# Kernel optimization log

Hardware: AMD Instinct MI355X
Metric: run time of the kernel (lower is better)

Reference implementation:

```python
import jax, jax.numpy as jnp
import numpy as np

NH = 16  # num_attention_heads
DH = 64  # attention_head_size
HS = 1024
LN_EPS = 1e-5


def _linear(x, W, b):
    return jnp.einsum('bsh,oh->bso', x, W) + b


def _mha(q, k, v, mask):
    # q:[B,Sq,H] k,v:[B,Sk,H] mask:[B,Sk] int (1=keep,0=mask)
    B, Sq, _ = q.shape
    Sk = k.shape[1]
    qh = q.reshape(B, Sq, NH, DH).transpose(0, 2, 1, 3)
    kh = k.reshape(B, Sk, NH, DH).transpose(0, 2, 1, 3)
    vh = v.reshape(B, Sk, NH, DH).transpose(0, 2, 1, 3)
    scores = jnp.einsum('bhqd,bhkd->bhqk', qh, kh) / np.sqrt(DH).astype(np.float32)
    if mask is not None:
        scores = jnp.where(mask[:, None, None, :] == 0, jnp.float32(-1e9), scores)
    probs = jax.nn.softmax(scores, axis=-1)  # dropout is identity in eval
    ctx = jnp.einsum('bhqk,bhkd->bhqd', probs, vh)
    return ctx.transpose(0, 2, 1, 3).reshape(B, Sq, NH * DH)


def _layernorm(x, g, b):
    mu = jnp.mean(x, axis=-1, keepdims=True)
    var = jnp.mean(jnp.square(x - mu), axis=-1, keepdims=True)
    return (x - mu) * jax.lax.rsqrt(var + LN_EPS) * g + b


def setup_inputs() -> dict:
    key = jax.random.key(0)
    ks = jax.random.split(key, 20)
    B, Sc, Se = 4, 512, 2048
    s = 0.02
    inp = {
        'claim_embeddings': jax.random.normal(ks[0], (B, Sc, HS), jnp.float32),
        'evidence_embeddings': jax.random.normal(ks[1], (B, Se, HS), jnp.float32),
        'claim_mask': jax.random.randint(ks[2], (B, Sc), 0, 2, jnp.int32),
        'evidence_mask': jax.random.randint(ks[3], (B, Se), 0, 2, jnp.int32),
    }
    names = ['cq', 'ek', 'ev', 'eq', 'ck', 'cv']
    for i, n in enumerate(names):
        inp['W_' + n] = jax.random.normal(ks[4 + i], (HS, HS), jnp.float32) * s
        inp['b_' + n] = jnp.zeros((HS,), jnp.float32)
    inp['ln_g'] = jnp.ones((HS,), jnp.float32)
    inp['ln_b'] = jnp.zeros((HS,), jnp.float32)
    return inp


def reference(claim_embeddings, evidence_embeddings, claim_mask, evidence_mask,
              W_cq, b_cq, W_ek, b_ek, W_ev, b_ev,
              W_eq, b_eq, W_ck, b_ck, W_cv, b_cv, ln_g, ln_b):
    claim_att = _mha(_linear(claim_embeddings, W_cq, b_cq),
                     _linear(evidence_embeddings, W_ek, b_ek),
                     _linear(evidence_embeddings, W_ev, b_ev), evidence_mask)
    evid_att = _mha(_linear(evidence_embeddings, W_eq, b_eq),
                    _linear(claim_embeddings, W_ck, b_ck),
                    _linear(claim_embeddings, W_cv, b_cv), claim_mask)
    claim_out = _layernorm(claim_embeddings + claim_att, ln_g, ln_b)
    evid_out = _layernorm(evidence_embeddings + evid_att, ln_g, ln_b)
    return (claim_out, evid_out)
```

## Files before the change

kernel.cpp:

```cpp
#include <hip/hip_runtime.h>
#include <hip/hip_bf16.h>
#include <stdint.h>

typedef __hip_bfloat16 bf16;
typedef __attribute__((ext_vector_type(8))) short bf16x8;
typedef __attribute__((ext_vector_type(4))) float f32x4;

#define DEV __device__ __forceinline__

DEV float lo_bf(unsigned int v) { union { unsigned int u; float f; } c; c.u = v << 16; return c.f; }
DEV float hi_bf(unsigned int v) { union { unsigned int u; float f; } c; c.u = v & 0xffff0000u; return c.f; }

DEV int probe_bf16(const void* ln_g) { return ((const uint16_t*)ln_g)[0] == 0x3F80; }

DEV unsigned short f2bs(float f) { union { bf16 h; unsigned short s; } u; u.h = __float2bfloat16(f); return u.s; }

DEV float ldf(const void* p, size_t i, int bfm) {
    return bfm ? __bfloat162float(((const bf16*)p)[i]) : ((const float*)p)[i];
}

DEV bf16x8 pack8(float4 x, float4 y) {
    union { unsigned short s[8]; bf16x8 v; } u;
    u.s[0] = f2bs(x.x); u.s[1] = f2bs(x.y); u.s[2] = f2bs(x.z); u.s[3] = f2bs(x.w);
    u.s[4] = f2bs(y.x); u.s[5] = f2bs(y.y); u.s[6] = f2bs(y.z); u.s[7] = f2bs(y.w);
    return u.v;
}

DEV bf16x8 ld8cvt(const void* p, size_t i, int bfm) {
    if (bfm) return *(const bf16x8*)((const bf16*)p + i);
    const float4* f = (const float4*)((const float*)p + i);
    return pack8(f[0], f[1]);
}

DEV void gload_lds16(const bf16* g, bf16* l) {
    __builtin_amdgcn_global_load_lds(
        (const __attribute__((address_space(1))) void*)g,
        (__attribute__((address_space(3))) void*)l,
        16, 0, 0);
}

__global__ __launch_bounds__(256) void conv_bf16(
    const void* __restrict__ Xc, const void* __restrict__ Xe,
    const void* __restrict__ W0, const void* __restrict__ W1, const void* __restrict__ W2,
    const void* __restrict__ W3, const void* __restrict__ W4, const void* __restrict__ W5,
    bf16* __restrict__ dst, const void* __restrict__ probe)
{
    const int bfm = probe_bf16(probe);
    const size_t tot = (size_t)16384 * 1024;
    const size_t step = (size_t)gridDim.x * 256 * 8;
    for (size_t e = ((size_t)blockIdx.x * 256 + threadIdx.x) * 8; e < tot; e += step) {
        const size_t row = e >> 10;
        const void* src; size_t off;
        if (row < 2048)       { src = Xc; off = e; }
        else if (row < 10240) { src = Xe; off = e - (size_t)2048 * 1024; }
        else {
            const int wi = (int)((row - 10240) >> 10);
            src = (wi == 0) ? W0 : (wi == 1) ? W1 : (wi == 2) ? W2 :
                  (wi == 3) ? W3 : (wi == 4) ? W4 : W5;
            off = e - (size_t)(10240 + wi * 1024) * 1024;
        }
        *(bf16x8*)(dst + e) = ld8cvt(src, off, bfm);
    }
}

__global__ __launch_bounds__(256) void gemm_fast(
    const bf16* __restrict__ AW,
    const void* __restrict__ B0, const void* __restrict__ B1, const void* __restrict__ B2,
    const void* __restrict__ B3, const void* __restrict__ B4, const void* __restrict__ B5,
    bf16* __restrict__ Out, const void* __restrict__ probe)
{
    __shared__ __align__(16) bf16 As[2][128 * 32];
    __shared__ __align__(16) bf16 Bs[2][128 * 32];

    const int bfm = probe_bf16(probe);
    const int L = (blockIdx.x & 7) * 240 + (blockIdx.x >> 3);
    const int z  = L / 640;
    const int rem = L % 640;
    const int bx = rem >> 3;
    const int by = rem & 7;
    const int rowBase = bx * 128;
    const int colBase = by * 128;
    const int ev = rowBase >= 2048;
    const int widx = z * 2 + ev;

    const bf16* Ap = AW;
    const bf16* Wp = AW + (size_t)(10240 + widx * 1024) * 1024;
    const void* bias = (widx == 0) ? B0 : (widx == 1) ? B1 : (widx == 2) ? B2 :
                       (widx == 3) ? B3 : (widx == 4) ? B4 : B5;
    bf16* O = Out + (size_t)z * 10240 * 1024;

    const int tid  = threadIdx.x;
    const int wave = tid >> 6;
    const int lane = tid & 63;
    const int wm   = wave >> 1;
    const int wn   = wave & 1;
    const int quad = lane >> 4;
    const int l16  = lane & 15;

    f32x4 acc[4][4];
#pragma unroll
    for (int i = 0; i < 4; i++)
#pragma unroll
        for (int j = 0; j < 4; j++) acc[i][j] = (f32x4){0.f, 0.f, 0.f, 0.f};

    const int sr = tid >> 2;
    const int sc = (tid & 3) * 8;
    const size_t ga = (size_t)(rowBase + sr) * 1024 + sc;
    const size_t gb = (size_t)(colBase + sr) * 1024 + sc;

    auto stage = [&](int buf, int k0) {
        gload_lds16(Ap + ga + k0,                     &As[buf][tid * 8]);
        gload_lds16(Ap + ga + (size_t)64 * 1024 + k0, &As[buf][2048 + tid * 8]);
        gload_lds16(Wp + gb + k0,                     &Bs[buf][tid * 8]);
        gload_lds16(Wp + gb + (size_t)64 * 1024 + k0, &Bs[buf][2048 + tid * 8]);
    };

    stage(0, 0);
    __syncthreads();

    int cur = 0;
    for (int k0 = 0; k0 < 1024; k0 += 32) {
        if (k0 + 32 < 1024) stage(cur ^ 1, k0 + 32);

        bf16x8 af[4], bfr[4];
#pragma unroll
        for (int i = 0; i < 4; i++) {
            af[i]  = *(const bf16x8*)(&As[cur][(wm * 64 + i * 16 + l16) * 32 + quad * 8]);
            bfr[i] = *(const bf16x8*)(&Bs[cur][(wn * 64 + i * 16 + l16) * 32 + quad * 8]);
        }
#pragma unroll
        for (int i = 0; i < 4; i++)
#pragma unroll
            for (int j = 0; j < 4; j++)
                acc[i][j] = __builtin_amdgcn_mfma_f32_16x16x32_bf16(af[i], bfr[j], acc[i][j], 0, 0, 0);

        __syncthreads();
        cur ^= 1;
    }

#pragma unroll
    for (int j = 0; j < 4; j++) {
        const int col = colBase + wn * 64 + j * 16 + l16;
        const float bv = ldf(bias, col, bfm);
#pragma unroll
        for (int i = 0; i < 4; i++) {
            const int row0 = rowBase + wm * 64 + i * 16 + quad * 4;
#pragma unroll
            for (int rr = 0; rr < 4; rr++)
                O[(size_t)(row0 + rr) * 1024 + col] = __float2bfloat16(acc[i][j][rr] + bv);
        }
    }
}

DEV void attn_core(const bf16* __restrict__ Q, const bf16* __restrict__ K,
                   const bf16* __restrict__ V, const int* __restrict__ mask,
                   bf16* __restrict__ O, int Sk, int h, int qRow0)
{
    __shared__ __align__(16) short Ks [64 * 72];
    __shared__ __align__(16) short VTs[64 * 72];
    __shared__ __align__(16) short Ps [4][16 * 72];

    const int tid  = threadIdx.x;
    const int w    = tid >> 6;
    const int lane = tid & 63;
    const int quad = lane >> 4;
    const int l16  = lane & 15;
    const int qRow = qRow0 + w * 16 + l16;

    const short* Qp = (const short*)Q + (size_t)qRow * 1024 + h * 64;
    const bf16x8 qf0 = *(const bf16x8*)(Qp + quad * 8);
    const bf16x8 qf1 = *(const bf16x8*)(Qp + 32 + quad * 8);

    f32x4 oacc[4];
#pragma unroll
    for (int dt = 0; dt < 4; dt++) oacc[dt] = (f32x4){0.f, 0.f, 0.f, 0.f};
    float mrun[4] = {-3e38f, -3e38f, -3e38f, -3e38f};
    float lrun[4] = {0.f, 0.f, 0.f, 0.f};

    const int sn = tid >> 2, sseg = tid & 3;
    const int vn = lane,     vdg  = w;

    bf16x8 pk0, pk1, pv0, pv1;
    auto loadkv = [&](int k0) {
        const short* src = (const short*)K + (size_t)(k0 + sn) * 1024 + h * 64 + sseg * 16;
        pk0 = *(const bf16x8*)src;
        pk1 = *(const bf16x8*)(src + 8);
        const short* vsrc = (const short*)V + (size_t)(k0 + vn) * 1024 + h * 64 + vdg * 16;
        pv0 = *(const bf16x8*)vsrc;
        pv1 = *(const bf16x8*)(vsrc + 8);
    };
    loadkv(0);

    for (int k0 = 0; k0 < Sk; k0 += 64) {
        __syncthreads();
        *(bf16x8*)(Ks + sn * 72 + sseg * 16)     = pk0;
        *(bf16x8*)(Ks + sn * 72 + sseg * 16 + 8) = pk1;
#pragma unroll
        for (int i = 0; i < 8; i++) VTs[(vdg * 16 + i) * 72 + vn]     = pv0[i];
#pragma unroll
        for (int i = 0; i < 8; i++) VTs[(vdg * 16 + 8 + i) * 72 + vn] = pv1[i];
        __syncthreads();
        {
            int kn = k0 + 64; if (kn >= Sk) kn = 0;
            loadkv(kn);
        }

        const int mv_all = mask[k0 + lane];

        f32x4 sacc[4];
#pragma unroll
        for (int t = 0; t < 4; t++) {
            const bf16x8 kf0 = *(const bf16x8*)(Ks + (t * 16 + l16) * 72 + quad * 8);
            const bf16x8 kf1 = *(const bf16x8*)(Ks + (t * 16 + l16) * 72 + 32 + quad * 8);
            f32x4 s = (f32x4){0.f, 0.f, 0.f, 0.f};
            s = __builtin_amdgcn_mfma_f32_16x16x32_bf16(qf0, kf0, s, 0, 0, 0);
            s = __builtin_amdgcn_mfma_f32_16x16x32_bf16(qf1, kf1, s, 0, 0, 0);
            const int mv = __shfl(mv_all, t * 16 + l16);
#pragma unroll
            for (int r = 0; r < 4; r++) sacc[t][r] = mv ? s[r] * 0.125f : -1e9f;
        }

        float cmax[4];
#pragma unroll
        for (int r = 0; r < 4; r++)
            cmax[r] = fmaxf(fmaxf(sacc[0][r], sacc[1][r]), fmaxf(sacc[2][r], sacc[3][r]));
#pragma unroll
        for (int m = 1; m < 16; m <<= 1)
#pragma unroll
            for (int r = 0; r < 4; r++) cmax[r] = fmaxf(cmax[r], __shfl_xor(cmax[r], m));

        float alpha[4], rsum[4];
#pragma unroll
        for (int r = 0; r < 4; r++) {
            const float mn = fmaxf(mrun[r], cmax[r]);
            alpha[r] = __expf(mrun[r] - mn);
            mrun[r] = mn;
            rsum[r] = 0.f;
        }
#pragma unroll
        for (int t = 0; t < 4; t++)
#pragma unroll
            for (int r = 0; r < 4; r++) {
                const float p = __expf(sacc[t][r] - mrun[r]);
                rsum[r] += p;
                Ps[w][(quad * 4 + r) * 72 + t * 16 + l16] = f2bs(p);
            }
#pragma unroll
        for (int m = 1; m < 16; m <<= 1)
#pragma unroll
            for (int r = 0; r < 4; r++) rsum[r] += __shfl_xor(rsum[r], m);
#pragma unroll
        for (int r = 0; r < 4; r++) lrun[r] = lrun[r] * alpha[r] + rsum[r];
#pragma unroll
        for (int dt = 0; dt < 4; dt++)
#pragma unroll
            for (int r = 0; r < 4; r++) oacc[dt][r] *= alpha[r];


        const bf16x8 pa0 = *(const bf16x8*)(Ps[w] + l16 * 72 + quad * 8);
        const bf16x8 pa1 = *(const bf16x8*)(Ps[w] + l16 * 72 + 32 + quad * 8);
#pragma unroll
        for (int dt = 0; dt < 4; dt++) {
            const bf16x8 vb0 = *(const bf16x8*)(VTs + (dt * 16 + l16) * 72 + quad * 8);
            const bf16x8 vb1 = *(const bf16x8*)(VTs + (dt * 16 + l16) * 72 + 32 + quad * 8);
            oacc[dt] = __builtin_amdgcn_mfma_f32_16x16x32_bf16(pa0, vb0, oacc[dt], 0, 0, 0);
            oacc[dt] = __builtin_amdgcn_mfma_f32_16x16x32_bf16(pa1, vb1, oacc[dt], 0, 0, 0);
        }
    }

    short* Op = (short*)O;
#pragma unroll
    for (int r = 0; r < 4; r++) {
        const float inv = 1.0f / lrun[r];
        const size_t row = (size_t)(qRow0 + w * 16 + quad * 4 + r) * 1024 + h * 64;
#pragma unroll
        for (int dt = 0; dt < 4; dt++)
            Op[row + dt * 16 + l16] = f2bs(oacc[dt][r] * inv);
    }
}

__global__ __launch_bounds__(256) void attn_flat(
    const bf16* __restrict__ Q1, const bf16* __restrict__ K1, const bf16* __restrict__ V1,
    const int* __restrict__ m1, bf16* __restrict__ O1,
    const bf16* __restrict__ Q2, const bf16* __restrict__ K2, const bf16* __restrict__ V2,
    const int* __restrict__ m2, bf16* __restrict__ O2)
{
    const int xcd = blockIdx.x & 7;
    const int idx = blockIdx.x >> 3;
    const int grp = idx / 5;
    const int pos = idx % 5;

    if (pos == 0) {
        const int j = xcd * 64 + grp;
        const int b = j >> 7;
        const int h = (j >> 3) & 15;
        const int qRow0 = (j & 7) * 64;
        attn_core(Q1 + (size_t)b * 512 * 1024,
                  K1 + (size_t)b * 2048 * 1024,
                  V1 + (size_t)b * 2048 * 1024,
                  m1 + (size_t)b * 2048,
                  O1 + (size_t)b * 512 * 1024, 2048, h, qRow0);
    } else {
        const int j = xcd * 256 + grp * 4 + (pos - 1);
        const int b = j >> 9;
        const int h = (j >> 5) & 15;
        const int qRow0 = (j & 31) * 64;
        attn_core(Q2 + (size_t)b * 2048 * 1024,
                  K2 + (size_t)b * 512 * 1024,
                  V2 + (size_t)b * 512 * 1024,
                  m2 + (size_t)b * 512,
                  O2 + (size_t)b * 2048 * 1024, 512, h, qRow0);
    }
}

__global__ __launch_bounds__(256) void attn_dual(
    const bf16* __restrict__ Q1, const bf16* __restrict__ K1, const bf16* __restrict__ V1,
    const int* __restrict__ m1, bf16* __restrict__ O1,
    const bf16* __restrict__ Q2, const bf16* __restrict__ K2, const bf16* __restrict__ V2,
    const int* __restrict__ m2, bf16* __restrict__ O2)
{
    const int z = blockIdx.z;
    if (z < 4) {
        if (blockIdx.x >= 8) return;
        attn_core(Q1 + (size_t)z * 512 * 1024,
                  K1 + (size_t)z * 2048 * 1024,
                  V1 + (size_t)z * 2048 * 1024,
                  m1 + (size_t)z * 2048,
                  O1 + (size_t)z * 512 * 1024, 2048, blockIdx.y, blockIdx.x * 64);
    } else {
        const int b = z - 4;
        attn_core(Q2 + (size_t)b * 2048 * 1024,
                  K2 + (size_t)b * 512 * 1024,
                  V2 + (size_t)b * 512 * 1024,
                  m2 + (size_t)b * 512,
                  O2 + (size_t)b * 2048 * 1024, 512, blockIdx.y, blockIdx.x * 64);
    }
}

DEV void gemm_core(const void* __restrict__ A, int aRow0,
                   const void* __restrict__ W, const void* __restrict__ bias,
                   bf16* __restrict__ O, int bfm)
{
    __shared__ __align__(16) short As [128 * 40];
    __shared__ __align__(16) short Bsh[128 * 40];

    const int tid  = threadIdx.x;
    const int wave = tid >> 6;
    const int lane = tid & 63;
    const int wm   = wave >> 1;
    const int wn   = wave & 1;
    const int quad = lane >> 4;
    const int l16  = lane & 15;

    const int rowBase = blockIdx.x * 128;
    const int colBase = blockIdx.y * 128;

    f32x4 acc[4][4];
#pragma unroll
    for (int i = 0; i < 4; i++)
#pragma unroll
        for (int j = 0; j < 4; j++) acc[i][j] = (f32x4){0.f, 0.f, 0.f, 0.f};

    const int r  = tid >> 2;
    const int c8 = (tid & 3) * 8;
    const size_t aIdx = (size_t)(aRow0 + rowBase + r) * 1024 + c8;
    const size_t wIdx = (size_t)(colBase + r) * 1024 + c8;
    short* sA0 = As  + r * 40 + c8;
    short* sA1 = As  + (r + 64) * 40 + c8;
    short* sB0 = Bsh + r * 40 + c8;
    short* sB1 = Bsh + (r + 64) * 40 + c8;

    auto compute = [&]() {
        bf16x8 af[4], bfr[4];
#pragma unroll
        for (int i = 0; i < 4; i++) {
            af[i]  = *(const bf16x8*)(As  + (wm * 64 + i * 16 + l16) * 40 + quad * 8);
            bfr[i] = *(const bf16x8*)(Bsh + (wn * 64 + i * 16 + l16) * 40 + quad * 8);
        }
#pragma unroll
        for (int i = 0; i < 4; i++)
#pragma unroll
            for (int j = 0; j < 4; j++)
                acc[i][j] = __builtin_amdgcn_mfma_f32_16x16x32_bf16(af[i], bfr[j], acc[i][j], 0, 0, 0);
    };

    if (bfm) {
        const bf16* Ab = (const bf16*)A;
        const bf16* Wb = (const bf16*)W;
        bf16x8 ra0 = *(const bf16x8*)(Ab + aIdx);
        bf16x8 ra1 = *(const bf16x8*)(Ab + aIdx + (size_t)64 * 1024);
        bf16x8 rb0 = *(const bf16x8*)(Wb + wIdx);
        bf16x8 rb1 = *(const bf16x8*)(Wb + wIdx + (size_t)64 * 1024);
        for (int k0 = 0; k0 < 1024; k0 += 32) {
            __syncthreads();
            *(bf16x8*)sA0 = ra0; *(bf16x8*)sA1 = ra1;
            *(bf16x8*)sB0 = rb0; *(bf16x8*)sB1 = rb1;
            __syncthreads();
            const int kn = (k0 + 32) & 1023;
            ra0 = *(const bf16x8*)(Ab + aIdx + kn);
            ra1 = *(const bf16x8*)(Ab + aIdx + (size_t)64 * 1024 + kn);
            rb0 = *(const bf16x8*)(Wb + wIdx + kn);
            rb1 = *(const bf16x8*)(Wb + wIdx + (size_t)64 * 1024 + kn);
            compute();
        }
    } else {
        const float* Af = (const float*)A;
        const float* Wf = (const float*)W;
        float4 f[4][2];
        auto loadf = [&](int k) {
            f[0][0] = *(const float4*)(Af + aIdx + k);
            f[0][1] = *(const float4*)(Af + aIdx + k + 4);
            f[1][0] = *(const float4*)(Af + aIdx + (size_t)64 * 1024 + k);
            f[1][1] = *(const float4*)(Af + aIdx + (size_t)64 * 1024 + k + 4);
            f[2][0] = *(const float4*)(Wf + wIdx + k);
            f[2][1] = *(const float4*)(Wf + wIdx + k + 4);
            f[3][0] = *(const float4*)(Wf + wIdx + (size_t)64 * 1024 + k);
            f[3][1] = *(const float4*)(Wf + wIdx + (size_t)64 * 1024 + k + 4);
        };
        loadf(0);
        for (int k0 = 0; k0 < 1024; k0 += 32) {
            const bf16x8 ra0 = pack8(f[0][0], f[0][1]);
            const bf16x8 ra1 = pack8(f[1][0], f[1][1]);
            const bf16x8 rb0 = pack8(f[2][0], f[2][1]);
            const bf16x8 rb1 = pack8(f[3][0], f[3][1]);
            __syncthreads();
            *(bf16x8*)sA0 = ra0; *(bf16x8*)sA1 = ra1;
            *(bf16x8*)sB0 = rb0; *(bf16x8*)sB1 = rb1;
            __syncthreads();
            loadf((k0 + 32) & 1023);
            compute();
        }
    }

#pragma unroll
    for (int j = 0; j < 4; j++) {
        const int col = colBase + wn * 64 + j * 16 + l16;
        const float bv = ldf(bias, col, bfm);
#pragma unroll
        for (int i = 0; i < 4; i++) {
            const int row0 = rowBase + wm * 64 + i * 16 + quad * 4;
#pragma unroll
            for (int rr = 0; rr < 4; rr++)
                O[(size_t)(row0 + rr) * 1024 + col] = __float2bfloat16(acc[i][j][rr] + bv);
        }
    }
}

__global__ __launch_bounds__(256) void gemm_bt6(
    const void* __restrict__ Ac, const void* __restrict__ Ae,
    const void* __restrict__ W0, const void* __restrict__ W1, const void* __restrict__ W2,
    const void* __restrict__ W3, const void* __restrict__ W4, const void* __restrict__ W5,
    const void* __restrict__ B0, const void* __restrict__ B1, const void* __restrict__ B2,
    const void* __restrict__ B3, const void* __restrict__ B4, const void* __restrict__ B5,
    bf16* __restrict__ O0, bf16* __restrict__ O1, bf16* __restrict__ O2,
    bf16* __restrict__ O3, bf16* __restrict__ O4, bf16* __restrict__ O5,
    const void* __restrict__ dt_probe)
{
    const int z = blockIdx.z;
    if (z < 3 && blockIdx.x >= 16) return;
    const int bfm = probe_bf16(dt_probe);
    const void* A = (z < 3) ? Ac : Ae;
    const void* W    = (z == 0) ? W0 : (z == 1) ? W1 : (z == 2) ? W2 : (z == 3) ? W3 : (z == 4) ? W4 : W5;
    const void* bias = (z == 0) ? B0 : (z == 1) ? B1 : (z == 2) ? B2 : (z == 3) ? B3 : (z == 4) ? B4 : B5;
    bf16* O          = (z == 0) ? O0 : (z == 1) ? O1 : (z == 2) ? O2 : (z == 3) ? O3 : (z == 4) ? O4 : O5;
    gemm_core(A, 0, W, bias, O, bfm);
}

DEV void ln_body(const void* __restrict__ X, size_t xrow, const bf16* __restrict__ Att,
                 size_t arow, const void* __restrict__ G, const void* __restrict__ Bb,
                 void* __restrict__ O, size_t orow, int bfm)
{
    __shared__ float r1[4], r2[4];
    const int tid = threadIdx.x;
    const size_t abase = arow * 1024 + tid * 4;
    const size_t xbase = xrow * 1024 + tid * 4;
    const uint2 ab = *(const uint2*)(Att + abase);
    const float v0 = ldf(X, xbase + 0, bfm) + lo_bf(ab.x);
    const float v1 = ldf(X, xbase + 1, bfm) + hi_bf(ab.x);
    const float v2 = ldf(X, xbase + 2, bfm) + lo_bf(ab.y);
    const float v3 = ldf(X, xbase + 3, bfm) + hi_bf(ab.y);
    float s  = v0 + v1 + v2 + v3;
    float ss = v0 * v0 + v1 * v1 + v2 * v2 + v3 * v3;
    for (int off = 32; off > 0; off >>= 1) { s += __shfl_down(s, off); ss += __shfl_down(ss, off); }
    if ((tid & 63) == 0) { r1[tid >> 6] = s; r2[tid >> 6] = ss; }
    __syncthreads();
    const float S  = r1[0] + r1[1] + r1[2] + r1[3];
    const float SS = r2[0] + r2[1] + r2[2] + r2[3];
    const float mu   = S * (1.f / 1024.f);
    const float var  = SS * (1.f / 1024.f) - mu * mu;
    const float rstd = rsqrtf(var + 1e-5f);
    const float g0 = ldf(G, tid * 4 + 0, bfm), g1 = ldf(G, tid * 4 + 1, bfm);
    const float g2 = ldf(G, tid * 4 + 2, bfm), g3 = ldf(G, tid * 4 + 3, bfm);
    const float bb0 = ldf(Bb, tid * 4 + 0, bfm), bb1 = ldf(Bb, tid * 4 + 1, bfm);
    const float bb2 = ldf(Bb, tid * 4 + 2, bfm), bb3 = ldf(Bb, tid * 4 + 3, bfm);
    const float o0 = (v0 - mu) * rstd * g0 + bb0;
    const float o1 = (v1 - mu) * rstd * g1 + bb1;
    const float o2 = (v2 - mu) * rstd * g2 + bb2;
    const float o3 = (v3 - mu) * rstd * g3 + bb3;
    const size_t obase = orow * 1024 + tid * 4;
    if (bfm) {
        union { unsigned short s4[4]; uint2 u; } pack;
        pack.s4[0] = f2bs(o0); pack.s4[1] = f2bs(o1); pack.s4[2] = f2bs(o2); pack.s4[3] = f2bs(o3);
        *(uint2*)((bf16*)O + obase) = pack.u;
    } else {
        *(float4*)((float*)O + obase) = (float4){o0, o1, o2, o3};
    }
}

__global__ __launch_bounds__(256) void ln_all(
    const void* __restrict__ Xc, const void* __restrict__ Xe, const bf16* __restrict__ Att,
    const void* __restrict__ G, const void* __restrict__ Bb, void* __restrict__ O)
{
    const int bfm = probe_bf16(G);
    const size_t row = blockIdx.x;
    if (row < 2048) ln_body(Xc, row,        Att, row, G, Bb, O, row, bfm);
    else            ln_body(Xe, row - 2048, Att, row, G, Bb, O, row, bfm);
}

__global__ __launch_bounds__(256) void ln_kernel(
    const void* __restrict__ X, int xRow0, const bf16* __restrict__ Att,
    const void* __restrict__ G, const void* __restrict__ Bb,
    void* __restrict__ O, size_t oRow0)
{
    const int bfm = probe_bf16(G);
    const size_t row = blockIdx.x;
    ln_body(X, (size_t)xRow0 + row, Att, row, G, Bb, O, oRow0 + row, bfm);
}

extern "C" void kernel_launch(void* const* d_in, const int* in_sizes, int n_in,
                              void* d_out, int out_size, void* d_ws, size_t ws_size,
                              hipStream_t stream)
{
    (void)in_sizes; (void)n_in; (void)out_size;

    const void* c_emb  = d_in[0];
    const void* e_emb  = d_in[1];
    const int*  c_mask = (const int*)d_in[2];
    const int*  e_mask = (const int*)d_in[3];
    const void* W_cq = d_in[4];  const void* b_cq = d_in[5];
    const void* W_ek = d_in[6];  const void* b_ek = d_in[7];
    const void* W_ev = d_in[8];  const void* b_ev = d_in[9];
    const void* W_eq = d_in[10]; const void* b_eq = d_in[11];
    const void* W_ck = d_in[12]; const void* b_ck = d_in[13];
    const void* W_cv = d_in[14]; const void* b_cv = d_in[15];
    const void* ln_g = d_in[16]; const void* ln_b = d_in[17];

    const int B = 4, Scl = 512, Sev = 2048;
    const size_t MC = (size_t)B * Scl;
    const size_t ME = (size_t)B * Sev;
    const size_t MT = MC + ME;
    const size_t RW = MT * 1024;

    dim3 blk(256);
    const size_t need_fast = (3 * RW + (size_t)16384 * 1024) * sizeof(bf16);

    if (ws_size >= need_fast) {
        bf16* Qr = (bf16*)d_ws;
        bf16* Kr = Qr + RW;
        bf16* Vr = Kr + RW;
        bf16* CV = Vr + RW;

        conv_bf16<<<dim3(2048), blk, 0, stream>>>(
            c_emb, e_emb, W_cq, W_eq, W_ck, W_ek, W_cv, W_ev, CV, ln_g);

        gemm_fast<<<dim3(1920), blk, 0, stream>>>(
            CV, b_cq, b_eq, b_ck, b_ek, b_cv, b_ev, Qr, ln_g);

        attn_flat<<<dim3(2560), blk, 0, stream>>>(
            Qr,             Kr + MC * 1024, Vr + MC * 1024, e_mask, Qr,
            Qr + MC * 1024, Kr,             Vr,             c_mask, Qr + MC * 1024);

        ln_all<<<dim3((unsigned)MT), blk, 0, stream>>>(
            c_emb, e_emb, Qr, ln_g, ln_b, d_out);
    } else {
        bf16* q_c = (bf16*)d_ws;
        bf16* k_c = q_c + MC * 1024;
        bf16* v_c = k_c + MC * 1024;
        bf16* q_e = v_c + MC * 1024;
        bf16* k_e = q_e + ME * 1024;
        bf16* v_e = k_e + ME * 1024;

        gemm_bt6<<<dim3(64, 8, 6), blk, 0, stream>>>(
            c_emb, e_emb,
            W_cq, W_ck, W_cv, W_eq, W_ek, W_ev,
            b_cq, b_ck, b_cv, b_eq, b_ek, b_ev,
            q_c, k_c, v_c, q_e, k_e, v_e, ln_g);

        attn_dual<<<dim3(32, 16, 8), blk, 0, stream>>>(
            q_c, k_e, v_e, e_mask, q_c,
            q_e, k_c, v_c, c_mask, q_e);

        ln_kernel<<<dim3((unsigned)MC), blk, 0, stream>>>(
            c_emb, 0, q_c, ln_g, ln_b, d_out, 0);
        ln_kernel<<<dim3((unsigned)ME), blk, 0, stream>>>(
            e_emb, 0, q_e, ln_g, ln_b, d_out, MC);
    }
}
```

Baseline: 431.3 us.

## Double-buffer K/V tiles in attention and fold softmax scale into exp2

The attention inner loop now ping-pongs between two shared-memory K and V^T buffers. The next tile is staged after the current PV matmul, so each iteration needs one barrier instead of two. The mask load is prefetched alongside K and V, and the 1/sqrt(d) scale is multiplied by log2(e) so the softmax can use exp2f instead of __expf. The cost is double the K/V LDS footprint, which may lower occupancy.

New measurement: 439.4 us. No clear change (+1.9%).

```diff
diff --git a/kernel.cpp b/kernel.cpp
--- a/kernel.cpp
+++ b/kernel.cpp
@@ -156,8 +156,8 @@
                    const bf16* __restrict__ V, const int* __restrict__ mask,
                    bf16* __restrict__ O, int Sk, int h, int qRow0)
 {
-    __shared__ __align__(16) short Ks [64 * 72];
-    __shared__ __align__(16) short VTs[64 * 72];
+    __shared__ __align__(16) short Ks [2][64 * 72];
+    __shared__ __align__(16) short VTs[2][64 * 72];
     __shared__ __align__(16) short Ps [4][16 * 72];
 
     const int tid  = threadIdx.x;
@@ -181,6 +181,7 @@
     const int vn = lane,     vdg  = w;
 
     bf16x8 pk0, pk1, pv0, pv1;
+    int pm;
     auto loadkv = [&](int k0) {
         const short* src = (const short*)K + (size_t)(k0 + sn) * 1024 + h * 64 + sseg * 16;
         pk0 = *(const bf16x8*)src;
@@ -188,36 +189,40 @@
         const short* vsrc = (const short*)V + (size_t)(k0 + vn) * 1024 + h * 64 + vdg * 16;
         pv0 = *(const bf16x8*)vsrc;
         pv1 = *(const bf16x8*)(vsrc + 8);
+        pm  = mask[k0 + lane];
     };
+    auto stage = [&](int buf) {
+        *(bf16x8*)(Ks[buf] + sn * 72 + sseg * 16)     = pk0;
+        *(bf16x8*)(Ks[buf] + sn * 72 + sseg * 16 + 8) = pk1;
+#pragma unroll
+        for (int i = 0; i < 8; i++) VTs[buf][(vdg * 16 + i) * 72 + vn]     = pv0[i];
+#pragma unroll
+        for (int i = 0; i < 8; i++) VTs[buf][(vdg * 16 + 8 + i) * 72 + vn] = pv1[i];
+    };
+
     loadkv(0);
-
+    stage(0);
+    __syncthreads();
+
+    const float SCL = 0.18033688f;
+
+    int cur = 0;
     for (int k0 = 0; k0 < Sk; k0 += 64) {
-        __syncthreads();
-        *(bf16x8*)(Ks + sn * 72 + sseg * 16)     = pk0;
-        *(bf16x8*)(Ks + sn * 72 + sseg * 16 + 8) = pk1;
-#pragma unroll
-        for (int i = 0; i < 8; i++) VTs[(vdg * 16 + i) * 72 + vn]     = pv0[i];
-#pragma unroll
-        for (int i = 0; i < 8; i++) VTs[(vdg * 16 + 8 + i) * 72 + vn] = pv1[i];
-        __syncthreads();
-        {
-            int kn = k0 + 64; if (kn >= Sk) kn = 0;
-            loadkv(kn);
-        }
-
-        const int mv_all = mask[k0 + lane];
+        const int mv_all = pm;
+        const bool more = (k0 + 64 < Sk);
+        if (more) loadkv(k0 + 64);
 
         f32x4 sacc[4];
 #pragma unroll
         for (int t = 0; t < 4; t++) {
-            const bf16x8 kf0 = *(const bf16x8*)(Ks + (t * 16 + l16) * 72 + quad * 8);
-            const bf16x8 kf1 = *(const bf16x8*)(Ks + (t * 16 + l16) * 72 + 32 + quad * 8);
+            const bf16x8 kf0 = *(const bf16x8*)(Ks[cur] + (t * 16 + l16) * 72 + quad * 8);
+            const bf16x8 kf1 = *(const bf16x8*)(Ks[cur] + (t * 16 + l16) * 72 + 32 + quad * 8);
             f32x4 s = (f32x4){0.f, 0.f, 0.f, 0.f};
             s = __builtin_amdgcn_mfma_f32_16x16x32_bf16(qf0, kf0, s, 0, 0, 0);
             s = __builtin_amdgcn_mfma_f32_16x16x32_bf16(qf1, kf1, s, 0, 0, 0);
             const int mv = __shfl(mv_all, t * 16 + l16);
 #pragma unroll
-            for (int r = 0; r < 4; r++) sacc[t][r] = mv ? s[r] * 0.125f : -1e9f;
+            for (int r = 0; r < 4; r++) sacc[t][r] = mv ? s[r] * SCL : -1e9f;
         }
 
         float cmax[4];
@@ -233,7 +238,7 @@
 #pragma unroll
         for (int r = 0; r < 4; r++) {
             const float mn = fmaxf(mrun[r], cmax[r]);
-            alpha[r] = __expf(mrun[r] - mn);
+            alpha[r] = exp2f(mrun[r] - mn);
             mrun[r] = mn;
             rsum[r] = 0.f;
         }
@@ -241,7 +246,7 @@
         for (int t = 0; t < 4; t++)
 #pragma unroll
             for (int r = 0; r < 4; r++) {
-                const float p = __expf(sacc[t][r] - mrun[r]);
+                const float p = exp2f(sacc[t][r] - mrun[r]);
                 rsum[r] += p;
                 Ps[w][(quad * 4 + r) * 72 + t * 16 + l16] = f2bs(p);
             }
@@ -261,10 +266,16 @@
         const bf16x8 pa1 = *(const bf16x8*)(Ps[w] + l16 * 72 + 32 + quad * 8);
 #pragma unroll
         for (int dt = 0; dt < 4; dt++) {
-            const bf16x8 vb0 = *(const bf16x8*)(VTs + (dt * 16 + l16) * 72 + quad * 8);
-            const bf16x8 vb1 = *(const bf16x8*)(VTs + (dt * 16 + l16) * 72 + 32 + quad * 8);
+            const bf16x8 vb0 = *(const bf16x8*)(VTs[cur] + (dt * 16 + l16) * 72 + quad * 8);
+            const bf16x8 vb1 = *(const bf16x8*)(VTs[cur] + (dt * 16 + l16) * 72 + 32 + quad * 8);
             oacc[dt] = __builtin_amdgcn_mfma_f32_16x16x32_bf16(pa0, vb0, oacc[dt], 0, 0, 0);
             oacc[dt] = __builtin_amdgcn_mfma_f32_16x16x32_bf16(pa1, vb1, oacc[dt], 0, 0, 0);
+        }
+
+        if (more) {
+            stage(cur ^ 1);
+            __syncthreads();
+            cur ^= 1;
         }
     }
 
```

## Process two query tiles per attention block to reuse staged K/V

Applied to the files above, without the earlier changes.

Adds attn_core2, in which each 256-thread block handles 128 query rows (two 64-row tiles per head) and reuses each K/V tile staged in shared memory for both. The flat attention grid is halved and its block-to-work mapping recomputed. This cuts global K/V loads and the shared-memory transpose work per query row, at the cost of more registers (doubled accumulators and softmax state) and fewer blocks to fill the GPU.

New measurement: 454.3 us. 5.3% more time.

```diff
diff --git a/kernel.cpp b/kernel.cpp
--- a/kernel.cpp
+++ b/kernel.cpp
@@ -152,30 +152,39 @@
     }
 }
 
-DEV void attn_core(const bf16* __restrict__ Q, const bf16* __restrict__ K,
-                   const bf16* __restrict__ V, const int* __restrict__ mask,
-                   bf16* __restrict__ O, int Sk, int h, int qRow0)
+DEV void attn_core2(const bf16* __restrict__ Q, const bf16* __restrict__ K,
+                    const bf16* __restrict__ V, const int* __restrict__ mask,
+                    bf16* __restrict__ O, int Sk, int h, int qRow0)
 {
     __shared__ __align__(16) short Ks [64 * 72];
     __shared__ __align__(16) short VTs[64 * 72];
-    __shared__ __align__(16) short Ps [4][16 * 72];
+    __shared__ __align__(16) short Ps [4][2][16 * 72];
 
     const int tid  = threadIdx.x;
     const int w    = tid >> 6;
     const int lane = tid & 63;
     const int quad = lane >> 4;
     const int l16  = lane & 15;
-    const int qRow = qRow0 + w * 16 + l16;
-
-    const short* Qp = (const short*)Q + (size_t)qRow * 1024 + h * 64;
-    const bf16x8 qf0 = *(const bf16x8*)(Qp + quad * 8);
-    const bf16x8 qf1 = *(const bf16x8*)(Qp + 32 + quad * 8);
-
-    f32x4 oacc[4];
-#pragma unroll
-    for (int dt = 0; dt < 4; dt++) oacc[dt] = (f32x4){0.f, 0.f, 0.f, 0.f};
-    float mrun[4] = {-3e38f, -3e38f, -3e38f, -3e38f};
-    float lrun[4] = {0.f, 0.f, 0.f, 0.f};
+
+    bf16x8 qf[2][2];
+#pragma unroll
+    for (int mt = 0; mt < 2; mt++) {
+        const short* Qp = (const short*)Q +
+            (size_t)(qRow0 + mt * 64 + w * 16 + l16) * 1024 + h * 64;
+        qf[mt][0] = *(const bf16x8*)(Qp + quad * 8);
+        qf[mt][1] = *(const bf16x8*)(Qp + 32 + quad * 8);
+    }
+
+    f32x4 oacc[2][4];
+    float mrun[2][4], lrun[2][4];
+#pragma unroll
+    for (int mt = 0; mt < 2; mt++)
+#pragma unroll
+        for (int dt = 0; dt < 4; dt++) {
+            oacc[mt][dt] = (f32x4){0.f, 0.f, 0.f, 0.f};
+            mrun[mt][dt] = -3e38f;
+            lrun[mt][dt] = 0.f;
+        }
 
     const int sn = tid >> 2, sseg = tid & 3;
     const int vn = lane,     vdg  = w;
@@ -207,6 +216,183 @@
 
         const int mv_all = mask[k0 + lane];
 
+        f32x4 sacc[2][4];
+#pragma unroll
+        for (int t = 0; t < 4; t++) {
+            const bf16x8 kf0 = *(const bf16x8*)(Ks + (t * 16 + l16) * 72 + quad * 8);
+            const bf16x8 kf1 = *(const bf16x8*)(Ks + (t * 16 + l16) * 72 + 32 + quad * 8);
+            const int mv = __shfl(mv_all, t * 16 + l16);
+#pragma unroll
+            for (int mt = 0; mt < 2; mt++) {
+                f32x4 s = (f32x4){0.f, 0.f, 0.f, 0.f};
+                s = __builtin_amdgcn_mfma_f32_16x16x32_bf16(qf[mt][0], kf0, s, 0, 0, 0);
+                s = __builtin_amdgcn_mfma_f32_16x16x32_bf16(qf[mt][1], kf1, s, 0, 0, 0);
+#pragma unroll
+                for (int r = 0; r < 4; r++) sacc[mt][t][r] = mv ? s[r] * 0.125f : -1e9f;
+            }
+        }
+
+#pragma unroll
+        for (int mt = 0; mt < 2; mt++) {
+            float cmax[4];
+#pragma unroll
+            for (int r = 0; r < 4; r++)
+                cmax[r] = fmaxf(fmaxf(sacc[mt][0][r], sacc[mt][1][r]),
+                                fmaxf(sacc[mt][2][r], sacc[mt][3][r]));
+#pragma unroll
+            for (int m = 1; m < 16; m <<= 1)
+#pragma unroll
+                for (int r = 0; r < 4; r++) cmax[r] = fmaxf(cmax[r], __shfl_xor(cmax[r], m));
+
+            float alpha[4], rsum[4];
+#pragma unroll
+            for (int r = 0; r < 4; r++) {
+                const float mn = fmaxf(mrun[mt][r], cmax[r]);
+                alpha[r] = __expf(mrun[mt][r] - mn);
+                mrun[mt][r] = mn;
+                rsum[r] = 0.f;
+            }
+#pragma unroll
+            for (int t = 0; t < 4; t++)
+#pragma unroll
+                for (int r = 0; r < 4; r++) {
+                    const float p = __expf(sacc[mt][t][r] - mrun[mt][r]);
+                    rsum[r] += p;
+                    Ps[w][mt][(quad * 4 + r) * 72 + t * 16 + l16] = f2bs(p);
+                }
+#pragma unroll
+            for (int m = 1; m < 16; m <<= 1)
+#pragma unroll
+                for (int r = 0; r < 4; r++) rsum[r] += __shfl_xor(rsum[r], m);
+#pragma unroll
+            for (int r = 0; r < 4; r++) lrun[mt][r] = lrun[mt][r] * alpha[r] + rsum[r];
+#pragma unroll
+            for (int dt = 0; dt < 4; dt++)
+#pragma unroll
+                for (int r = 0; r < 4; r++) oacc[mt][dt][r] *= alpha[r];
+        }
+
+
+        bf16x8 pa[2][2];
+#pragma unroll
+        for (int mt = 0; mt < 2; mt++) {
+            pa[mt][0] = *(const bf16x8*)(Ps[w][mt] + l16 * 72 + quad * 8);
+            pa[mt][1] = *(const bf16x8*)(Ps[w][mt] + l16 * 72 + 32 + quad * 8);
+        }
+#pragma unroll
+        for (int dt = 0; dt < 4; dt++) {
+            const bf16x8 vb0 = *(const bf16x8*)(VTs + (dt * 16 + l16) * 72 + quad * 8);
+            const bf16x8 vb1 = *(const bf16x8*)(VTs + (dt * 16 + l16) * 72 + 32 + quad * 8);
+#pragma unroll
+            for (int mt = 0; mt < 2; mt++) {
+                oacc[mt][dt] = __builtin_amdgcn_mfma_f32_16x16x32_bf16(pa[mt][0], vb0, oacc[mt][dt], 0, 0, 0);
+                oacc[mt][dt] = __builtin_amdgcn_mfma_f32_16x16x32_bf16(pa[mt][1], vb1, oacc[mt][dt], 0, 0, 0);
+            }
+        }
+    }
+
+    short* Op = (short*)O;
+#pragma unroll
+    for (int mt = 0; mt < 2; mt++)
+#pragma unroll
+        for (int r = 0; r < 4; r++) {
+            const float inv = 1.0f / lrun[mt][r];
+            const size_t row = (size_t)(qRow0 + mt * 64 + w * 16 + quad * 4 + r) * 1024 + h * 64;
+#pragma unroll
+            for (int dt = 0; dt < 4; dt++)
+                Op[row + dt * 16 + l16] = f2bs(oacc[mt][dt][r] * inv);
+        }
+}
+
+__global__ __launch_bounds__(256) void attn_flat(
+    const bf16* __restrict__ Q1, const bf16* __restrict__ K1, const bf16* __restrict__ V1,
+    const int* __restrict__ m1, bf16* __restrict__ O1,
+    const bf16* __restrict__ Q2, const bf16* __restrict__ K2, const bf16* __restrict__ V2,
+    const int* __restrict__ m2, bf16* __restrict__ O2)
+{
+    const int xcd = blockIdx.x & 7;
+    const int idx = blockIdx.x >> 3;
+    const int grp = idx / 5;
+    const int pos = idx % 5;
+
+    if (pos == 0) {
+        const int j = xcd * 32 + grp;
+        const int b = j >> 6;
+        const int h = (j >> 2) & 15;
+        const int qRow0 = (j & 3) * 128;
+        attn_core2(Q1 + (size_t)b * 512 * 1024,
+                   K1 + (size_t)b * 2048 * 1024,
+                   V1 + (size_t)b * 2048 * 1024,
+                   m1 + (size_t)b * 2048,
+                   O1 + (size_t)b * 512 * 1024, 2048, h, qRow0);
+    } else {
+        const int j = xcd * 128 + grp * 4 + (pos - 1);
+        const int b = j >> 8;
+        const int h = (j >> 4) & 15;
+        const int qRow0 = (j & 15) * 128;
+        attn_core2(Q2 + (size_t)b * 2048 * 1024,
+                   K2 + (size_t)b * 512 * 1024,
+                   V2 + (size_t)b * 512 * 1024,
+                   m2 + (size_t)b * 512,
+                   O2 + (size_t)b * 2048 * 1024, 512, h, qRow0);
+    }
+}
+
+DEV void attn_core(const bf16* __restrict__ Q, const bf16* __restrict__ K,
+                   const bf16* __restrict__ V, const int* __restrict__ mask,
+                   bf16* __restrict__ O, int Sk, int h, int qRow0)
+{
+    __shared__ __align__(16) short Ks [64 * 72];
+    __shared__ __align__(16) short VTs[64 * 72];
+    __shared__ __align__(16) short Ps [4][16 * 72];
+
+    const int tid  = threadIdx.x;
+    const int w    = tid >> 6;
+    const int lane = tid & 63;
+    const int quad = lane >> 4;
+    const int l16  = lane & 15;
+    const int qRow = qRow0 + w * 16 + l16;
+
+    const short* Qp = (const short*)Q + (size_t)qRow * 1024 + h * 64;
+    const bf16x8 qf0 = *(const bf16x8*)(Qp + quad * 8);
+    const bf16x8 qf1 = *(const bf16x8*)(Qp + 32 + quad * 8);
+
+    f32x4 oacc[4];
+#pragma unroll
+    for (int dt = 0; dt < 4; dt++) oacc[dt] = (f32x4){0.f, 0.f, 0.f, 0.f};
+    float mrun[4] = {-3e38f, -3e38f, -3e38f, -3e38f};
+    float lrun[4] = {0.f, 0.f, 0.f, 0.f};
+
+    const int sn = tid >> 2, sseg = tid & 3;
+    const int vn = lane,     vdg  = w;
+
+    bf16x8 pk0, pk1, pv0, pv1;
+    auto loadkv = [&](int k0) {
+        const short* src = (const short*)K + (size_t)(k0 + sn) * 1024 + h * 64 + sseg * 16;
+        pk0 = *(const bf16x8*)src;
+        pk1 = *(const bf16x8*)(src + 8);
+        const short* vsrc = (const short*)V + (size_t)(k0 + vn) * 1024 + h * 64 + vdg * 16;
+        pv0 = *(const bf16x8*)vsrc;
+        pv1 = *(const bf16x8*)(vsrc + 8);
+    };
+    loadkv(0);
+
+    for (int k0 = 0; k0 < Sk; k0 += 64) {
+        __syncthreads();
+        *(bf16x8*)(Ks + sn * 72 + sseg * 16)     = pk0;
+        *(bf16x8*)(Ks + sn * 72 + sseg * 16 + 8) = pk1;
+#pragma unroll
+        for (int i = 0; i < 8; i++) VTs[(vdg * 16 + i) * 72 + vn]     = pv0[i];
+#pragma unroll
+        for (int i = 0; i < 8; i++) VTs[(vdg * 16 + 8 + i) * 72 + vn] = pv1[i];
+        __syncthreads();
+        {
+            int kn = k0 + 64; if (kn >= Sk) kn = 0;
+            loadkv(kn);
+        }
+
+        const int mv_all = mask[k0 + lane];
+
         f32x4 sacc[4];
 #pragma unroll
         for (int t = 0; t < 4; t++) {
@@ -256,7 +442,6 @@
 #pragma unroll
             for (int r = 0; r < 4; r++) oacc[dt][r] *= alpha[r];
 
-
         const bf16x8 pa0 = *(const bf16x8*)(Ps[w] + l16 * 72 + quad * 8);
         const bf16x8 pa1 = *(const bf16x8*)(Ps[w] + l16 * 72 + 32 + quad * 8);
 #pragma unroll
@@ -276,40 +461,6 @@
 #pragma unroll
         for (int dt = 0; dt < 4; dt++)
             Op[row + dt * 16 + l16] = f2bs(oacc[dt][r] * inv);
-    }
-}
-
-__global__ __launch_bounds__(256) void attn_flat(
-    const bf16* __restrict__ Q1, const bf16* __restrict__ K1, const bf16* __restrict__ V1,
-    const int* __restrict__ m1, bf16* __restrict__ O1,
-    const bf16* __restrict__ Q2, const bf16* __restrict__ K2, const bf16* __restrict__ V2,
-    const int* __restrict__ m2, bf16* __restrict__ O2)
-{
-    const int xcd = blockIdx.x & 7;
-    const int idx = blockIdx.x >> 3;
-    const int grp = idx / 5;
-    const int pos = idx % 5;
-
-    if (pos == 0) {
-        const int j = xcd * 64 + grp;
-        const int b = j >> 7;
-        const int h = (j >> 3) & 15;
-        const int qRow0 = (j & 7) * 64;
-        attn_core(Q1 + (size_t)b * 512 * 1024,
-                  K1 + (size_t)b * 2048 * 1024,
-                  V1 + (size_t)b * 2048 * 1024,
-                  m1 + (size_t)b * 2048,
-                  O1 + (size_t)b * 512 * 1024, 2048, h, qRow0);
-    } else {
-        const int j = xcd * 256 + grp * 4 + (pos - 1);
-        const int b = j >> 9;
-        const int h = (j >> 5) & 15;
-        const int qRow0 = (j & 31) * 64;
-        attn_core(Q2 + (size_t)b * 2048 * 1024,
-                  K2 + (size_t)b * 512 * 1024,
-                  V2 + (size_t)b * 512 * 1024,
-                  m2 + (size_t)b * 512,
-                  O2 + (size_t)b * 2048 * 1024, 512, h, qRow0);
     }
 }
 
@@ -566,7 +717,7 @@
         gemm_fast<<<dim3(1920), blk, 0, stream>>>(
             CV, b_cq, b_eq, b_ck, b_ek, b_cv, b_ev, Qr, ln_g);
 
-        attn_flat<<<dim3(2560), blk, 0, stream>>>(
+        attn_flat<<<dim3(1280), blk, 0, stream>>>(
             Qr,             Kr + MC * 1024, Vr + MC * 1024, e_mask, Qr,
             Qr + MC * 1024, Kr,             Vr,             c_mask, Qr + MC * 1024);
 
```

## Pack V-transpose LDS stores as pairs and use wave-per-row layernorm

Applied to the files above, without the earlier changes.

The attention kernel now has each thread load V from two adjacent key rows and write packed 32-bit pairs into the transposed V tile, replacing 16 scattered 16-bit LDS stores with 8 32-bit stores. Separately, the layernorm is rewritten so one wavefront handles a whole row with 16 elements per lane and xor-shuffle reductions. This drops the block-level shared-memory reduction and its barriers and gives wider vectorized loads. The single-pass variance (E[x^2]-mu^2) may lose a little precision.

Measured after the change: 413.8 us. 1.04x faster.

```diff
diff --git a/kernel.cpp b/kernel.cpp
--- a/kernel.cpp
+++ b/kernel.cpp
@@ -10,6 +10,7 @@
 
 DEV float lo_bf(unsigned int v) { union { unsigned int u; float f; } c; c.u = v << 16; return c.f; }
 DEV float hi_bf(unsigned int v) { union { unsigned int u; float f; } c; c.u = v & 0xffff0000u; return c.f; }
+DEV float bs2f(short h) { union { unsigned int u; float f; } c; c.u = ((unsigned int)(unsigned short)h) << 16; return c.f; }
 
 DEV int probe_bf16(const void* ln_g) { return ((const uint16_t*)ln_g)[0] == 0x3F80; }
 
@@ -178,16 +179,17 @@
     float lrun[4] = {0.f, 0.f, 0.f, 0.f};
 
     const int sn = tid >> 2, sseg = tid & 3;
-    const int vn = lane,     vdg  = w;
+    const int vn2 = (tid & 31) * 2;
+    const int vdg = tid >> 5;
 
     bf16x8 pk0, pk1, pv0, pv1;
     auto loadkv = [&](int k0) {
         const short* src = (const short*)K + (size_t)(k0 + sn) * 1024 + h * 64 + sseg * 16;
         pk0 = *(const bf16x8*)src;
         pk1 = *(const bf16x8*)(src + 8);
-        const short* vsrc = (const short*)V + (size_t)(k0 + vn) * 1024 + h * 64 + vdg * 16;
+        const short* vsrc = (const short*)V + (size_t)(k0 + vn2) * 1024 + h * 64 + vdg * 8;
         pv0 = *(const bf16x8*)vsrc;
-        pv1 = *(const bf16x8*)(vsrc + 8);
+        pv1 = *(const bf16x8*)(vsrc + 1024);
     };
     loadkv(0);
 
@@ -196,9 +198,11 @@
         *(bf16x8*)(Ks + sn * 72 + sseg * 16)     = pk0;
         *(bf16x8*)(Ks + sn * 72 + sseg * 16 + 8) = pk1;
 #pragma unroll
-        for (int i = 0; i < 8; i++) VTs[(vdg * 16 + i) * 72 + vn]     = pv0[i];
-#pragma unroll
-        for (int i = 0; i < 8; i++) VTs[(vdg * 16 + 8 + i) * 72 + vn] = pv1[i];
+        for (int i = 0; i < 8; i++) {
+            const unsigned int pr = (unsigned short)pv0[i] |
+                                    ((unsigned int)(unsigned short)pv1[i] << 16);
+            *(unsigned int*)(VTs + (vdg * 8 + i) * 72 + vn2) = pr;
+        }
         __syncthreads();
         {
             int kn = k0 + 64; if (kn >= Sk) kn = 0;
@@ -464,6 +468,96 @@
     const void* bias = (z == 0) ? B0 : (z == 1) ? B1 : (z == 2) ? B2 : (z == 3) ? B3 : (z == 4) ? B4 : B5;
     bf16* O          = (z == 0) ? O0 : (z == 1) ? O1 : (z == 2) ? O2 : (z == 3) ? O3 : (z == 4) ? O4 : O5;
     gemm_core(A, 0, W, bias, O, bfm);
+}
+
+__global__ __launch_bounds__(256) void ln_wave(
+    const void* __restrict__ Xc, const void* __restrict__ Xe, const bf16* __restrict__ Att,
+    const void* __restrict__ G, const void* __restrict__ Bb, void* __restrict__ O)
+{
+    const int bfm = probe_bf16(G);
+    const int lane = threadIdx.x & 63;
+    const size_t row = (size_t)blockIdx.x * 4 + (threadIdx.x >> 6);
+    const void* X; size_t xrow;
+    if (row < 2048) { X = Xc; xrow = row; }
+    else            { X = Xe; xrow = row - 2048; }
+
+    const int e0 = lane * 16;
+    float v[16];
+    {
+        const short* ap = (const short*)Att + row * 1024 + e0;
+        const bf16x8 a0 = *(const bf16x8*)ap;
+        const bf16x8 a1 = *(const bf16x8*)(ap + 8);
+#pragma unroll
+        for (int j = 0; j < 8; j++) { v[j] = bs2f(a0[j]); v[8 + j] = bs2f(a1[j]); }
+    }
+    if (bfm) {
+        const short* xp = (const short*)X + xrow * 1024 + e0;
+        const bf16x8 x0 = *(const bf16x8*)xp;
+        const bf16x8 x1 = *(const bf16x8*)(xp + 8);
+#pragma unroll
+        for (int j = 0; j < 8; j++) { v[j] += bs2f(x0[j]); v[8 + j] += bs2f(x1[j]); }
+    } else {
+        const float* xp = (const float*)X + xrow * 1024 + e0;
+#pragma unroll
+        for (int q = 0; q < 4; q++) {
+            const float4 f = *(const float4*)(xp + q * 4);
+            v[q * 4 + 0] += f.x; v[q * 4 + 1] += f.y;
+            v[q * 4 + 2] += f.z; v[q * 4 + 3] += f.w;
+        }
+    }
+
+    float s = 0.f, ss = 0.f;
+#pragma unroll
+    for (int j = 0; j < 16; j++) { s += v[j]; ss += v[j] * v[j]; }
+#pragma unroll
+    for (int off = 32; off > 0; off >>= 1) {
+        s  += __shfl_xor(s,  off);
+        ss += __shfl_xor(ss, off);
+    }
+    const float mu   = s * (1.f / 1024.f);
+    const float var  = ss * (1.f / 1024.f) - mu * mu;
+    const float rstd = rsqrtf(var + 1e-5f);
+
+    float g[16], bb[16];
+    if (bfm) {
+        const short* gp = (const short*)G + e0;
+        const short* bp = (const short*)Bb + e0;
+        const bf16x8 g0 = *(const bf16x8*)gp, g1 = *(const bf16x8*)(gp + 8);
+        const bf16x8 b0 = *(const bf16x8*)bp, b1 = *(const bf16x8*)(bp + 8);
+#pragma unroll
+        for (int j = 0; j < 8; j++) {
+            g[j] = bs2f(g0[j]); g[8 + j] = bs2f(g1[j]);
+            bb[j] = bs2f(b0[j]); bb[8 + j] = bs2f(b1[j]);
+        }
+    } else {
+        const float* gp = (const float*)G + e0;
+        const float* bp = (const float*)Bb + e0;
+#pragma unroll
+        for (int q = 0; q < 4; q++) {
+            const float4 gf = *(const float4*)(gp + q * 4);
+            const float4 bf = *(const float4*)(bp + q * 4);
+            g[q * 4 + 0] = gf.x; g[q * 4 + 1] = gf.y; g[q * 4 + 2] = gf.z; g[q * 4 + 3] = gf.w;
+            bb[q * 4 + 0] = bf.x; bb[q * 4 + 1] = bf.y; bb[q * 4 + 2] = bf.z; bb[q * 4 + 3] = bf.w;
+        }
+    }
+
+    float o[16];
+#pragma unroll
+    for (int j = 0; j < 16; j++) o[j] = (v[j] - mu) * rstd * g[j] + bb[j];
+
+    const size_t obase = row * 1024 + e0;
+    if (bfm) {
+        union { unsigned short sh[16]; uint4 u[2]; } pk;
+#pragma unroll
+        for (int j = 0; j < 16; j++) pk.sh[j] = f2bs(o[j]);
+        uint4* op = (uint4*)((bf16*)O + obase);
+        op[0] = pk.u[0]; op[1] = pk.u[1];
+    } else {
+        float* op = (float*)O + obase;
+#pragma unroll
+        for (int q = 0; q < 4; q++)
+            *(float4*)(op + q * 4) = (float4){o[q * 4], o[q * 4 + 1], o[q * 4 + 2], o[q * 4 + 3]};
+    }
 }
 
 DEV void ln_body(const void* __restrict__ X, size_t xrow, const bf16* __restrict__ Att,
@@ -507,16 +601,6 @@
     }
 }
 
-__global__ __launch_bounds__(256) void ln_all(
-    const void* __restrict__ Xc, const void* __restrict__ Xe, const bf16* __restrict__ Att,
-    const void* __restrict__ G, const void* __restrict__ Bb, void* __restrict__ O)
-{
-    const int bfm = probe_bf16(G);
-    const size_t row = blockIdx.x;
-    if (row < 2048) ln_body(Xc, row,        Att, row, G, Bb, O, row, bfm);
-    else            ln_body(Xe, row - 2048, Att, row, G, Bb, O, row, bfm);
-}
-
 __global__ __launch_bounds__(256) void ln_kernel(
     const void* __restrict__ X, int xRow0, const bf16* __restrict__ Att,
     const void* __restrict__ G, const void* __restrict__ Bb,
@@ -570,7 +654,7 @@
             Qr,             Kr + MC * 1024, Vr + MC * 1024, e_mask, Qr,
             Qr + MC * 1024, Kr,             Vr,             c_mask, Qr + MC * 1024);
 
-        ln_all<<<dim3((unsigned)MT), blk, 0, stream>>>(
+        ln_wave<<<dim3((unsigned)(MT / 4)), blk, 0, stream>>>(
             c_emb, e_emb, Qr, ln_g, ln_b, d_out);
     } else {
         bf16* q_c = (bf16*)d_ws;
```
